# Performance work log

Measured on AMD Instinct MI355X. Metric: run time of the kernel, lower is better.

The kernel has to match this reference:

```python
import math
import jax, jax.numpy as jnp
import numpy as np

B, C, F, W_FRAMES = 1, 8, 1024, 512
H = 16                      # num_heads
D = F // H                  # head dim = 64
ROPE_DIM = D // 2           # 32: only first half of head dim is rotated
EXP = 4                     # ffn expansion
EPS = 1e-5
MAX_FREQ = 10.0             # rotary-embedding-torch default


def frame_norm(x, g, b):
    # LayerNorm over the feature axis (axis=2) of (b, c, F, w)
    mu = jnp.mean(x, axis=2, keepdims=True)
    var = jnp.mean(jnp.square(x - mu), axis=2, keepdims=True)
    xn = (x - mu) * jax.lax.rsqrt(var + EPS)
    return xn * g[None, None, :, None] + b[None, None, :, None]


def mc_linear(x, w_pw):
    # per-channel pointwise linear: out[b,c,f,w] = sum_g W[c,f,g] x[b,c,g,w]
    return jnp.einsum('bcgw,cfg->bcfw', x, w_pw)


def apply_rope(t, freqs_seq):
    # t: (b, c, H, w, d); freqs_seq: (w, rot_dim)
    rot_dim = freqs_seq.shape[-1]
    t_rot, t_pass = t[..., :rot_dim], t[..., rot_dim:]
    cos, sin = jnp.cos(freqs_seq), jnp.sin(freqs_seq)
    x1, x2 = t_rot[..., 0::2], t_rot[..., 1::2]
    rh = jnp.stack([-x2, x1], axis=-1).reshape(t_rot.shape)  # interleaved rotate_half
    return jnp.concatenate([t_rot * cos + rh * sin, t_pass], axis=-1)


def attention(x, w_q, w_o, rope_freqs):
    b, c, f, w = x.shape
    # NOTE: source uses q_proj for q, k AND v (k_proj/v_proj unused)
    p = mc_linear(x, w_q)                                    # (b,c,F,w)
    t = p.transpose(0, 1, 3, 2).reshape(b, c, w, H, D).transpose(0, 1, 3, 2, 4)  # (b,c,H,w,d)
    pos = jnp.arange(w, dtype=t.dtype)
    freqs_seq = jnp.repeat(pos[:, None] * rope_freqs[None, :], 2, axis=-1)  # (w, rot_dim)
    q = apply_rope(t, freqs_seq)
    k = apply_rope(t, freqs_seq)
    v = t
    scores = jnp.einsum('bchqd,bchkd->bchqk', q, k) / math.sqrt(f)  # scaled by sqrt(features)!
    a = jax.nn.softmax(scores, axis=-1)
    o = jnp.einsum('bchqk,bchkd->bchqd', a, v)
    o = o.transpose(0, 1, 3, 2, 4).reshape(b, c, w, f).transpose(0, 1, 3, 2)  # (b,c,F,w)
    return mc_linear(o, w_o)


def setup_inputs() -> dict:
    key = jax.random.key(0)
    ks = jax.random.split(key, 8)
    s = 1.0 / math.sqrt(F)
    se = 1.0 / math.sqrt(F * EXP)
    x = jax.random.normal(ks[0], (B, C, F, W_FRAMES), dtype=jnp.float32)
    w_q = jax.random.uniform(ks[1], (C, F, F), jnp.float32, -s, s)
    w_o = jax.random.uniform(ks[2], (C, F, F), jnp.float32, -s, s)
    w1 = jax.random.uniform(ks[3], (C, F * EXP, F), jnp.float32, -s, s)
    w2 = jax.random.uniform(ks[4], (C, F, F * EXP), jnp.float32, -se, se)
    rope_freqs = jnp.linspace(1.0, MAX_FREQ / 2, ROPE_DIM // 2, dtype=jnp.float32) * math.pi
    return {
        'x': x,
        'norm1_g': jnp.ones((F,), jnp.float32), 'norm1_b': jnp.zeros((F,), jnp.float32),
        'w_q': w_q, 'w_o': w_o, 'rope_freqs': rope_freqs,
        'norm2_g': jnp.ones((F,), jnp.float32), 'norm2_b': jnp.zeros((F,), jnp.float32),
        'w1': w1, 'w2': w2,
    }


def reference(x, norm1_g, norm1_b, w_q, w_o, rope_freqs, norm2_g, norm2_b, w1, w2):
    # FrameTransformerEncoder, eval mode (dropout = identity)
    z = frame_norm(x, norm1_g, norm1_b)
    x = x + attention(z, w_q, w_o, rope_freqs)
    z = frame_norm(x, norm2_g, norm2_b)
    z = mc_linear(jax.nn.gelu(mc_linear(z, w1), approximate=False), w2)
    return x + z
```

## Files before the change

### kernel.cpp

```cpp
#include <hip/hip_runtime.h>
#include <math.h>

#define CC 8
#define FF 1024
#define WW 512
#define HH 16
#define DD 64
#define FE 4096
#define EPS_ 1e-5f

typedef __attribute__((ext_vector_type(8))) short bf16x8;
typedef __attribute__((ext_vector_type(4))) float f32x4;

static __device__ __forceinline__ unsigned short f2bf(float f) {
    unsigned u = __float_as_uint(f);
    u += 0x7fffu + ((u >> 16) & 1u);
    return (unsigned short)(u >> 16);
}
static __device__ __forceinline__ float bf2f(unsigned short h) {
    return __uint_as_float(((unsigned)h) << 16);
}
static __device__ __forceinline__ float gelu_exact(float v) {
    return 0.5f * v * (1.0f + erff(v * 0.70710678118654752f));
}
static __device__ __forceinline__ unsigned cvt_pk_bf16(float lo, float hi) {
    unsigned r;
    asm("v_cvt_pk_bf16_f32 %0, %1, %2" : "=v"(r) : "v"(lo), "v"(hi));
    return r;
}

typedef const __attribute__((address_space(1))) unsigned int* gas_p;
typedef __attribute__((address_space(3))) unsigned int* las_p;
static __device__ __forceinline__ void gload_lds16(const void* g, void* l) {
    __builtin_amdgcn_global_load_lds((gas_p)g, (las_p)l, 16, 0, 0);
}

__global__ __launch_bounds__(256) void fn_stats_k(
    const float* __restrict__ x, float2* __restrict__ part)
{
    int c  = blockIdx.z;
    int w0 = blockIdx.x * 64;
    int f0 = blockIdx.y * 128;
    int t  = threadIdx.x, wl = t & 63, fg = t >> 6;
    const float* xc = x + (size_t)c * FF * WW;

    float s = 0.f, q = 0.f;
    #pragma unroll 8
    for (int i = 0; i < 32; i++) {
        int f = f0 + fg + 4 * i;
        float v = xc[(size_t)f * WW + w0 + wl];
        s += v; q += v * v;
    }
    __shared__ float ss[4][64], sq_[4][64];
    ss[fg][wl] = s; sq_[fg][wl] = q;
    __syncthreads();
    if (fg == 0) {
        float S = 0.f, Q = 0.f;
        #pragma unroll
        for (int j = 0; j < 4; j++) { S += ss[j][wl]; Q += sq_[j][wl]; }
        part[((size_t)c * WW + w0 + wl) * 8 + blockIdx.y] = make_float2(S, Q);
    }
}

__global__ __launch_bounds__(256) void fn_apply_k(
    const float* __restrict__ x, const float2* __restrict__ part,
    const float* __restrict__ g, const float* __restrict__ b,
    unsigned short* __restrict__ zt)
{
    int c  = blockIdx.z;
    int w0 = blockIdx.x * 64;
    int f0 = blockIdx.y * 64;
    int t  = threadIdx.x, wl = t & 63, fg = t >> 6;

    __shared__ float smu[64], srv[64];
    __shared__ float sT[64][65];

    if (t < 64) {
        float S = 0.f, Q = 0.f;
        #pragma unroll
        for (int fs = 0; fs < 8; fs++) {
            float2 v = part[((size_t)c * WW + w0 + t) * 8 + fs];
            S += v.x; Q += v.y;
        }
        float mu  = S * (1.f / FF);
        float var = Q * (1.f / FF) - mu * mu;
        smu[t] = mu;
        srv[t] = rsqrtf(var + EPS_);
    }
    const float* xc = x + (size_t)c * FF * WW;
    #pragma unroll
    for (int i = 0; i < 16; i++) {
        int fl = fg * 16 + i;
        sT[fl][wl] = xc[(size_t)(f0 + fl) * WW + w0 + wl];
    }
    __syncthreads();

    unsigned short* ztc = zt + (size_t)c * WW * FF;
    float gv = g[f0 + wl], bv = b[f0 + wl];
    #pragma unroll
    for (int i = 0; i < 16; i++) {
        int wr = fg * 16 + i;
        ztc[(size_t)(w0 + wr) * FF + f0 + wl] =
            f2bf((sT[wl][wr] - smu[wr]) * srv[wr] * gv + bv);
    }
}

template<int BM, int MINW>
__global__ __launch_bounds__(256, MINW) void gemm_v6_k(
    const float* __restrict__ A, const unsigned short* __restrict__ Bt,
    float* __restrict__ Outf, unsigned short* __restrict__ Outb,
    const float* __restrict__ Add, int M, int K, int mode)
{
    constexpr int L  = BM / 16;
    constexpr int MI = BM / 32;
    constexpr int AP = 72;

    int bid = blockIdx.x;
    int c   = bid & 7;
    int rem = bid >> 3;
    int nt  = rem & 3;
    int mt  = rem >> 2;
    int m0  = mt * BM, n0 = nt * 128;
    const float*          Ac = A  + (size_t)c * M * K;
    const unsigned short* Bc = Bt + ((size_t)c * 512 + n0) * K;

    __shared__ unsigned short sA[2][BM * AP];
    __shared__ unsigned short sB[2][128 * 64];

    int t    = threadIdx.x;
    int lane = t & 63;
    int wid  = t >> 6;
    int frl  = lane & 15, fgr = lane >> 4;
    int WM   = (wid >> 1) * (MI * 16);
    int WN   = (wid & 1) * 64;

    f32x4 acc[MI][4];
    #pragma unroll
    for (int i = 0; i < MI; i++)
        #pragma unroll
        for (int j = 0; j < 4; j++) acc[i][j] = (f32x4){0.f, 0.f, 0.f, 0.f};

    int arow = t >> 4;
    int acol = (t & 15) * 4;
    float4 ar[L];

    int bro   = lane >> 3;
    int bslot = (lane & 7) ^ bro;

    auto loadA = [&](int k0) {
        #pragma unroll
        for (int p = 0; p < L; p++)
            ar[p] = *reinterpret_cast<const float4*>(
                Ac + (size_t)(m0 + p * 16 + arow) * K + k0 + acol);
    };
    auto cvtWriteA = [&](int buf) {
        #pragma unroll
        for (int p = 0; p < L; p++) {
            uint2 u;
            u.x = cvt_pk_bf16(ar[p].x, ar[p].y);
            u.y = cvt_pk_bf16(ar[p].z, ar[p].w);
            *reinterpret_cast<uint2*>(&sA[buf][(p * 16 + arow) * AP + acol]) = u;
        }
    };
    auto stageB = [&](int buf, int k0) {
        #pragma unroll
        for (int r = 0; r < 4; r++) {
            int rbase = wid * 32 + r * 8;
            gload_lds16(Bc + (size_t)(rbase + bro) * K + k0 + bslot * 8,
                        &sB[buf][rbase * 64]);
        }
    };

    loadA(0);
    asm volatile("s_waitcnt vmcnt(0)" ::: "memory");
    cvtWriteA(0);
    stageB(0, 0);

    int NT = K >> 6;
    for (int kt = 0; kt < NT; ++kt) {
        int  cur  = kt & 1;
        bool more = (kt + 1 < NT);

        if (more) loadA((kt + 1) << 6);
        if (more) {
            if constexpr (BM == 128)
                asm volatile("s_waitcnt vmcnt(8)" ::: "memory");
            else
                asm volatile("s_waitcnt vmcnt(4)" ::: "memory");
        } else {
            asm volatile("s_waitcnt vmcnt(0)" ::: "memory");
        }
        asm volatile("s_waitcnt lgkmcnt(0)" ::: "memory");
        __builtin_amdgcn_sched_barrier(0);
        __builtin_amdgcn_s_barrier();

        if (more) stageB(cur ^ 1, (kt + 1) << 6);

        #pragma unroll
        for (int ks = 0; ks < 2; ks++) {
            bf16x8 af[MI], bfv[4];
            #pragma unroll
            for (int mi = 0; mi < MI; mi++)
                af[mi] = *reinterpret_cast<const bf16x8*>(
                    &sA[cur][(WM + mi * 16 + frl) * AP + ks * 32 + fgr * 8]);
            #pragma unroll
            for (int ni = 0; ni < 4; ni++) {
                int row  = WN + ni * 16 + frl;
                int slot = ((ks << 2) | fgr) ^ (frl & 7);
                bfv[ni] = *reinterpret_cast<const bf16x8*>(
                    &sB[cur][row * 64 + slot * 8]);
            }
            #pragma unroll
            for (int mi = 0; mi < MI; mi++)
                #pragma unroll
                for (int ni = 0; ni < 4; ni++)
                    acc[mi][ni] = __builtin_amdgcn_mfma_f32_16x16x32_bf16(
                        af[mi], bfv[ni], acc[mi][ni], 0, 0, 0);
        }

        if (more) {
            asm volatile("s_waitcnt vmcnt(4)" ::: "memory");
            __builtin_amdgcn_sched_barrier(0);
            cvtWriteA(cur ^ 1);
        }
    }

    if (mode == 1) {
        #pragma unroll
        for (int mi = 0; mi < MI; mi++)
            #pragma unroll
            for (int ni = 0; ni < 4; ni++) {
                int mrow = m0 + WM + mi * 16 + fgr * 4;
                int ncol = n0 + WN + ni * 16 + frl;
                #pragma unroll
                for (int r = 0; r < 4; r++) {
                    size_t o = ((size_t)c * M + mrow + r) * 512 + ncol;
                    Outf[o] = acc[mi][ni][r] + Add[o];
                }
            }
    } else {
        bool gel = (mode == 2);
        #pragma unroll
        for (int mi = 0; mi < MI; mi++)
            #pragma unroll
            for (int ni = 0; ni < 4; ni++) {
                f32x4 v = acc[mi][ni];
                if (gel) {
                    v[0] = gelu_exact(v[0]); v[1] = gelu_exact(v[1]);
                    v[2] = gelu_exact(v[2]); v[3] = gelu_exact(v[3]);
                }
                int mrow = m0 + WM + mi * 16 + fgr * 4;
                int ncol = n0 + WN + ni * 16 + frl;
                ushort4 h;
                h.x = f2bf(v[0]); h.y = f2bf(v[1]);
                h.z = f2bf(v[2]); h.w = f2bf(v[3]);
                *reinterpret_cast<ushort4*>(
                    &Outb[((size_t)c * 512 + ncol) * M + mrow]) = h;
            }
    }
}

__global__ __launch_bounds__(256) void attn_mfma_k(
    const unsigned short* __restrict__ pt, const float* __restrict__ fr,
    unsigned short* __restrict__ ot)
{
    int ch = blockIdx.y;
    int c  = ch >> 4, h = ch & 15;
    int q0 = blockIdx.x * 64;
    int t  = threadIdx.x;
    int lane = t & 63;
    int wid  = t >> 6;
    int frl  = lane & 15, fgr = lane >> 4;

    const unsigned short* base = pt + (size_t)c * WW * FF + h * DD;

    __shared__ unsigned short Qs[64 * 72];
    __shared__ unsigned short Ks[64 * 72];
    __shared__ unsigned short Vt[64 * 72];
    __shared__ unsigned short Ps[4 * 16 * 72];

    {
        int kr = t >> 3, d0 = (t & 7) * 8;
        #pragma unroll
        for (int r = 0; r < 2; r++) {
            int row = kr + r * 32;
            int w   = q0 + row;
            bf16x8 v = *reinterpret_cast<const bf16x8*>(&base[(size_t)w * FF + d0]);
            bf16x8 o;
            if (d0 < 32) {
                #pragma unroll
                for (int j = 0; j < 8; j += 2) {
                    float x1 = bf2f((unsigned short)v[j]);
                    float x2 = bf2f((unsigned short)v[j + 1]);
                    float sn, cs;
                    __sincosf((float)w * fr[(d0 + j) >> 1], &sn, &cs);
                    o[j]     = (short)f2bf(x1 * cs - x2 * sn);
                    o[j + 1] = (short)f2bf(x2 * cs + x1 * sn);
                }
            } else o = v;
            *reinterpret_cast<bf16x8*>(&Qs[row * 72 + d0]) = o;
        }
    }

    f32x4 oacc[4];
    float m_[4], l_[4];
    #pragma unroll
    for (int i = 0; i < 4; i++) {
        oacc[i] = (f32x4){0.f, 0.f, 0.f, 0.f};
        m_[i] = -1e30f; l_[i] = 0.f;
    }
    unsigned short* myP = &Ps[wid * 16 * 72];
    int wq0 = wid * 16;

    for (int k0 = 0; k0 < WW; k0 += 64) {
        __syncthreads();
        {
            int kr = t >> 3, d0 = (t & 7) * 8;
            #pragma unroll
            for (int r = 0; r < 2; r++) {
                int row = kr + r * 32;
                int w   = k0 + row;
                bf16x8 v = *reinterpret_cast<const bf16x8*>(&base[(size_t)w * FF + d0]);
                bf16x8 o;
                if (d0 < 32) {
                    #pragma unroll
                    for (int j = 0; j < 8; j += 2) {
                        float x1 = bf2f((unsigned short)v[j]);
                        float x2 = bf2f((unsigned short)v[j + 1]);
                        float sn, cs;
                        __sincosf((float)w * fr[(d0 + j) >> 1], &sn, &cs);
                        o[j]     = (short)f2bf(x1 * cs - x2 * sn);
                        o[j + 1] = (short)f2bf(x2 * cs + x1 * sn);
                    }
                } else o = v;
                *reinterpret_cast<bf16x8*>(&Ks[row * 72 + d0]) = o;
            }
        }
        {
            int d  = t & 63;
            int kb = (t >> 6) * 8;
            #pragma unroll
            for (int r = 0; r < 2; r++) {
                int kk = kb + r * 32;
                bf16x8 o;
                #pragma unroll
                for (int j = 0; j < 8; j++)
                    o[j] = (short)base[(size_t)(k0 + kk + j) * FF + d];
                *reinterpret_cast<bf16x8*>(&Vt[d * 72 + kk]) = o;
            }
        }
        __syncthreads();

        f32x4 s[4];
        #pragma unroll
        for (int nt = 0; nt < 4; nt++) s[nt] = (f32x4){0.f, 0.f, 0.f, 0.f};
        bf16x8 aq0 = *reinterpret_cast<const bf16x8*>(&Qs[(wq0 + frl) * 72 + fgr * 8]);
        bf16x8 aq1 = *reinterpret_cast<const bf16x8*>(&Qs[(wq0 + frl) * 72 + 32 + fgr * 8]);
        #pragma unroll
        for (int nt = 0; nt < 4; nt++) {
            bf16x8 b0 = *reinterpret_cast<const bf16x8*>(&Ks[(nt * 16 + frl) * 72 + fgr * 8]);
            bf16x8 b1 = *reinterpret_cast<const bf16x8*>(&Ks[(nt * 16 + frl) * 72 + 32 + fgr * 8]);
            s[nt] = __builtin_amdgcn_mfma_f32_16x16x32_bf16(aq0, b0, s[nt], 0, 0, 0);
            s[nt] = __builtin_amdgcn_mfma_f32_16x16x32_bf16(aq1, b1, s[nt], 0, 0, 0);
        }

        #pragma unroll
        for (int r = 0; r < 4; r++) {
            float sv[4];
            #pragma unroll
            for (int nt = 0; nt < 4; nt++) sv[nt] = s[nt][r] * (1.f / 32.f);
            float mx = fmaxf(fmaxf(sv[0], sv[1]), fmaxf(sv[2], sv[3]));
            mx = fmaxf(mx, __shfl_xor(mx, 1, 64));
            mx = fmaxf(mx, __shfl_xor(mx, 2, 64));
            mx = fmaxf(mx, __shfl_xor(mx, 4, 64));
            mx = fmaxf(mx, __shfl_xor(mx, 8, 64));
            float mn    = fmaxf(m_[r], mx);
            float scale = __expf(m_[r] - mn);
            float rs = 0.f;
            #pragma unroll
            for (int nt = 0; nt < 4; nt++) {
                float p = __expf(sv[nt] - mn);
                myP[(fgr * 4 + r) * 72 + nt * 16 + frl] = f2bf(p);
                rs += p;
            }
            rs += __shfl_xor(rs, 1, 64);
            rs += __shfl_xor(rs, 2, 64);
            rs += __shfl_xor(rs, 4, 64);
            rs += __shfl_xor(rs, 8, 64);
            l_[r] = l_[r] * scale + rs;
            m_[r] = mn;
            #pragma unroll
            for (int dt = 0; dt < 4; dt++) oacc[dt][r] *= scale;
        }

        bf16x8 ap0 = *reinterpret_cast<const bf16x8*>(&myP[frl * 72 + fgr * 8]);
        bf16x8 ap1 = *reinterpret_cast<const bf16x8*>(&myP[frl * 72 + 32 + fgr * 8]);
        #pragma unroll
        for (int dt = 0; dt < 4; dt++) {
            bf16x8 b0 = *reinterpret_cast<const bf16x8*>(&Vt[(dt * 16 + frl) * 72 + fgr * 8]);
            bf16x8 b1 = *reinterpret_cast<const bf16x8*>(&Vt[(dt * 16 + frl) * 72 + 32 + fgr * 8]);
            oacc[dt] = __builtin_amdgcn_mfma_f32_16x16x32_bf16(ap0, b0, oacc[dt], 0, 0, 0);
            oacc[dt] = __builtin_amdgcn_mfma_f32_16x16x32_bf16(ap1, b1, oacc[dt], 0, 0, 0);
        }
    }

    unsigned short* ob = ot + (size_t)c * WW * FF + h * DD;
    #pragma unroll
    for (int r = 0; r < 4; r++) {
        float inv = 1.f / l_[r];
        int w = q0 + wq0 + fgr * 4 + r;
        #pragma unroll
        for (int dt = 0; dt < 4; dt++)
            ob[(size_t)w * FF + dt * 16 + frl] = f2bf(oacc[dt][r] * inv);
    }
}

extern "C" void kernel_launch(void* const* d_in, const int* in_sizes, int n_in,
                              void* d_out, int out_size, void* d_ws, size_t ws_size,
                              hipStream_t stream)
{
    const float* x  = (const float*)d_in[0];
    const float* g1 = (const float*)d_in[1];
    const float* b1 = (const float*)d_in[2];
    const float* wq = (const float*)d_in[3];
    const float* wo = (const float*)d_in[4];
    const float* fr = (const float*)d_in[5];
    const float* g2 = (const float*)d_in[6];
    const float* b2 = (const float*)d_in[7];
    const float* w1 = (const float*)d_in[8];
    const float* w2 = (const float*)d_in[9];

    const size_t SZ = (size_t)CC * FF * WW;
    char* wsb = (char*)d_ws;
    unsigned short* zt  = (unsigned short*)(wsb);
    unsigned short* ptb = (unsigned short*)(wsb + 2 * SZ);
    unsigned short* otb = (unsigned short*)(wsb + 4 * SZ);
    float*          x2  = (float*)        (wsb + 6 * SZ);
    unsigned short* h1t = (unsigned short*)(wsb + 10 * SZ);
    float2*         prt = (float2*)       (wsb + 18 * SZ);

    dim3 b256(256);
    dim3 gst(WW / 64, FF / 128, CC);
    dim3 gap(WW / 64, FF / 64, CC);

    fn_stats_k<<<gst, b256, 0, stream>>>(x, prt);
    fn_apply_k<<<gap, b256, 0, stream>>>(x, prt, g1, b1, zt);
    gemm_v6_k<64, 3><<<dim3(512), b256, 0, stream>>>(
        wq, zt, nullptr, ptb, nullptr, FF, FF, 0);
    attn_mfma_k<<<dim3(WW / 64, CC * HH), b256, 0, stream>>>(ptb, fr, otb);
    gemm_v6_k<64, 3><<<dim3(512), b256, 0, stream>>>(
        wo, otb, x2, nullptr, x, FF, FF, 1);
    fn_stats_k<<<gst, b256, 0, stream>>>(x2, prt);
    fn_apply_k<<<gap, b256, 0, stream>>>(x2, prt, g2, b2, zt);
    gemm_v6_k<128, 2><<<dim3(1024), b256, 0, stream>>>(
        w1, zt, nullptr, h1t, nullptr, FE, FF, 2);
    gemm_v6_k<64, 3><<<dim3(512), b256, 0, stream>>>(
        w2, h1t, (float*)d_out, nullptr, x2, FF, FE, 1);
}
```

Before: 265.1 us.

## Switch GEMM inner loop to 32x32x16 bf16 MFMA with XOR-swizzled A tile

Replaces the 16x16x32 MFMA tiling in the shared GEMM kernel with 32x32x16 bf16 MFMA instructions, so each wave computes larger fragments and issues fewer instructions and LDS fragment reads per unit of work. The padded A shared-memory tile (stride 72) becomes an unpadded stride-64 layout with an XOR swizzle that matches the B tile, which removes padding and is meant to avoid bank conflicts. The epilogue is rewritten for the 32x32 accumulator layout. The 16-float accumulators may raise register pressure, and the new output write pattern changes coalescing.

```diff
diff --git a/kernel.cpp b/kernel.cpp
--- a/kernel.cpp
+++ b/kernel.cpp
@@ -11,6 +11,7 @@
 
 typedef __attribute__((ext_vector_type(8))) short bf16x8;
 typedef __attribute__((ext_vector_type(4))) float f32x4;
+typedef __attribute__((ext_vector_type(16))) float f32x16;
 
 static __device__ __forceinline__ unsigned short f2bf(float f) {
     unsigned u = __float_as_uint(f);
@@ -106,14 +107,13 @@
 }
 
 template<int BM, int MINW>
-__global__ __launch_bounds__(256, MINW) void gemm_v6_k(
+__global__ __launch_bounds__(256, MINW) void gemm_v7_k(
     const float* __restrict__ A, const unsigned short* __restrict__ Bt,
     float* __restrict__ Outf, unsigned short* __restrict__ Outb,
     const float* __restrict__ Add, int M, int K, int mode)
 {
     constexpr int L  = BM / 16;
-    constexpr int MI = BM / 32;
-    constexpr int AP = 72;
+    constexpr int MF = BM / 64;
 
     int bid = blockIdx.x;
     int c   = bid & 7;
@@ -124,24 +124,28 @@
     const float*          Ac = A  + (size_t)c * M * K;
     const unsigned short* Bc = Bt + ((size_t)c * 512 + n0) * K;
 
-    __shared__ unsigned short sA[2][BM * AP];
+    __shared__ unsigned short sA[2][BM * 64];
     __shared__ unsigned short sB[2][128 * 64];
 
     int t    = threadIdx.x;
     int lane = t & 63;
     int wid  = t >> 6;
-    int frl  = lane & 15, fgr = lane >> 4;
-    int WM   = (wid >> 1) * (MI * 16);
+    int l31  = lane & 31, l5 = lane >> 5;
+    int r7   = l31 & 7;
+    int WM   = (wid >> 1) * (BM / 2);
     int WN   = (wid & 1) * 64;
 
-    f32x4 acc[MI][4];
+    f32x16 acc[MF][2];
     #pragma unroll
-    for (int i = 0; i < MI; i++)
-        #pragma unroll
-        for (int j = 0; j < 4; j++) acc[i][j] = (f32x4){0.f, 0.f, 0.f, 0.f};
+    for (int i = 0; i < MF; i++)
+        #pragma unroll
+        for (int j = 0; j < 2; j++)
+            #pragma unroll
+            for (int e = 0; e < 16; e++) acc[i][j][e] = 0.f;
 
     int arow = t >> 4;
     int acol = (t & 15) * 4;
+    int awz  = (((acol >> 3) ^ (arow & 7)) << 3) + (acol & 7);
     float4 ar[L];
 
     int bro   = lane >> 3;
@@ -159,7 +163,7 @@
             uint2 u;
             u.x = cvt_pk_bf16(ar[p].x, ar[p].y);
             u.y = cvt_pk_bf16(ar[p].z, ar[p].w);
-            *reinterpret_cast<uint2*>(&sA[buf][(p * 16 + arow) * AP + acol]) = u;
+            *reinterpret_cast<uint2*>(&sA[buf][(p * 16 + arow) * 64 + awz]) = u;
         }
     };
     auto stageB = [&](int buf, int k0) {
@@ -197,25 +201,23 @@
         if (more) stageB(cur ^ 1, (kt + 1) << 6);
 
         #pragma unroll
-        for (int ks = 0; ks < 2; ks++) {
-            bf16x8 af[MI], bfv[4];
-            #pragma unroll
-            for (int mi = 0; mi < MI; mi++)
-                af[mi] = *reinterpret_cast<const bf16x8*>(
-                    &sA[cur][(WM + mi * 16 + frl) * AP + ks * 32 + fgr * 8]);
-            #pragma unroll
-            for (int ni = 0; ni < 4; ni++) {
-                int row  = WN + ni * 16 + frl;
-                int slot = ((ks << 2) | fgr) ^ (frl & 7);
-                bfv[ni] = *reinterpret_cast<const bf16x8*>(
-                    &sB[cur][row * 64 + slot * 8]);
-            }
-            #pragma unroll
-            for (int mi = 0; mi < MI; mi++)
+        for (int ksf = 0; ksf < 4; ksf++) {
+            int gx = (((ksf * 2 + l5) ^ r7) << 3);
+            bf16x8 af[MF], bfv[2];
+            #pragma unroll
+            for (int mf = 0; mf < MF; mf++)
+                af[mf] = *reinterpret_cast<const bf16x8*>(
+                    &sA[cur][(WM + mf * 32 + l31) * 64 + gx]);
+            #pragma unroll
+            for (int nf = 0; nf < 2; nf++)
+                bfv[nf] = *reinterpret_cast<const bf16x8*>(
+                    &sB[cur][(WN + nf * 32 + l31) * 64 + gx]);
+            #pragma unroll
+            for (int mf = 0; mf < MF; mf++)
                 #pragma unroll
-                for (int ni = 0; ni < 4; ni++)
-                    acc[mi][ni] = __builtin_amdgcn_mfma_f32_16x16x32_bf16(
-                        af[mi], bfv[ni], acc[mi][ni], 0, 0, 0);
+                for (int nf = 0; nf < 2; nf++)
+                    acc[mf][nf] = __builtin_amdgcn_mfma_f32_32x32x16_bf16(
+                        af[mf], bfv[nf], acc[mf][nf], 0, 0, 0);
         }
 
         if (more) {
@@ -227,35 +229,44 @@
 
     if (mode == 1) {
         #pragma unroll
-        for (int mi = 0; mi < MI; mi++)
-            #pragma unroll
-            for (int ni = 0; ni < 4; ni++) {
-                int mrow = m0 + WM + mi * 16 + fgr * 4;
-                int ncol = n0 + WN + ni * 16 + frl;
+        for (int mf = 0; mf < MF; mf++)
+            #pragma unroll
+            for (int nf = 0; nf < 2; nf++) {
+                int ncol = n0 + WN + nf * 32 + l31;
+                int mb   = m0 + WM + mf * 32 + l5 * 4;
                 #pragma unroll
-                for (int r = 0; r < 4; r++) {
-                    size_t o = ((size_t)c * M + mrow + r) * 512 + ncol;
-                    Outf[o] = acc[mi][ni][r] + Add[o];
-                }
+                for (int g = 0; g < 4; g++)
+                    #pragma unroll
+                    for (int j = 0; j < 4; j++) {
+                        int row = mb + g * 8 + j;
+                        size_t o = ((size_t)c * M + row) * 512 + ncol;
+                        Outf[o] = acc[mf][nf][g * 4 + j] + Add[o];
+                    }
             }
     } else {
         bool gel = (mode == 2);
         #pragma unroll
-        for (int mi = 0; mi < MI; mi++)
-            #pragma unroll
-            for (int ni = 0; ni < 4; ni++) {
-                f32x4 v = acc[mi][ni];
-                if (gel) {
-                    v[0] = gelu_exact(v[0]); v[1] = gelu_exact(v[1]);
-                    v[2] = gelu_exact(v[2]); v[3] = gelu_exact(v[3]);
+        for (int mf = 0; mf < MF; mf++)
+            #pragma unroll
+            for (int nf = 0; nf < 2; nf++) {
+                int ncol = n0 + WN + nf * 32 + l31;
+                int mb   = m0 + WM + mf * 32 + l5 * 4;
+                #pragma unroll
+                for (int g = 0; g < 4; g++) {
+                    float v0 = acc[mf][nf][g * 4 + 0];
+                    float v1 = acc[mf][nf][g * 4 + 1];
+                    float v2 = acc[mf][nf][g * 4 + 2];
+                    float v3 = acc[mf][nf][g * 4 + 3];
+                    if (gel) {
+                        v0 = gelu_exact(v0); v1 = gelu_exact(v1);
+                        v2 = gelu_exact(v2); v3 = gelu_exact(v3);
+                    }
+                    ushort4 h;
+                    h.x = f2bf(v0); h.y = f2bf(v1);
+                    h.z = f2bf(v2); h.w = f2bf(v3);
+                    *reinterpret_cast<ushort4*>(
+                        &Outb[((size_t)c * 512 + ncol) * M + mb + g * 8]) = h;
                 }
-                int mrow = m0 + WM + mi * 16 + fgr * 4;
-                int ncol = n0 + WN + ni * 16 + frl;
-                ushort4 h;
-                h.x = f2bf(v[0]); h.y = f2bf(v[1]);
-                h.z = f2bf(v[2]); h.w = f2bf(v[3]);
-                *reinterpret_cast<ushort4*>(
-                    &Outb[((size_t)c * 512 + ncol) * M + mrow]) = h;
             }
     }
 }
@@ -445,15 +456,15 @@
 
     fn_stats_k<<<gst, b256, 0, stream>>>(x, prt);
     fn_apply_k<<<gap, b256, 0, stream>>>(x, prt, g1, b1, zt);
-    gemm_v6_k<64, 3><<<dim3(512), b256, 0, stream>>>(
+    gemm_v7_k<64, 3><<<dim3(512), b256, 0, stream>>>(
         wq, zt, nullptr, ptb, nullptr, FF, FF, 0);
     attn_mfma_k<<<dim3(WW / 64, CC * HH), b256, 0, stream>>>(ptb, fr, otb);
-    gemm_v6_k<64, 3><<<dim3(512), b256, 0, stream>>>(
+    gemm_v7_k<64, 3><<<dim3(512), b256, 0, stream>>>(
         wo, otb, x2, nullptr, x, FF, FF, 1);
     fn_stats_k<<<gst, b256, 0, stream>>>(x2, prt);
     fn_apply_k<<<gap, b256, 0, stream>>>(x2, prt, g2, b2, zt);
-    gemm_v6_k<128, 2><<<dim3(1024), b256, 0, stream>>>(
+    gemm_v7_k<128, 2><<<dim3(1024), b256, 0, stream>>>(
         w1, zt, nullptr, h1t, nullptr, FE, FF, 2);
-    gemm_v6_k<64, 3><<<dim3(512), b256, 0, stream>>>(
+    gemm_v7_k<64, 3><<<dim3(512), b256, 0, stream>>>(
         w2, h1t, (float*)d_out, nullptr, x2, FF, FE, 1);
 }
```

New measurement: 302.8 us. +14.2%, slower.

## Add dedicated 128x256-tile GEMM kernel for the W1 FFN projection

Applied to the files above, without the earlier changes.

Replaces the generic templated GEMM used for the first FFN layer with a specialized kernel that computes a 128x256 output tile per block (4 waves, each 64x128), halving the grid to 512 blocks. Each block loads fp32 weights, converts them to bf16 in registers, and double-buffers both operands in LDS, with B staged via direct global-to-LDS loads. The larger tile increases reuse of the weight and activation tiles, cutting global traffic per FLOP. In exchange it uses many accumulator registers (launch bounds of 2 blocks per CU) and fewer blocks, which may reduce occupancy and latency hiding.

```diff
diff --git a/kernel.cpp b/kernel.cpp
--- a/kernel.cpp
+++ b/kernel.cpp
@@ -258,6 +258,136 @@
                     &Outb[((size_t)c * 512 + ncol) * M + mrow]) = h;
             }
     }
+}
+
+__global__ __launch_bounds__(256, 2) void gemm_w1big_k(
+    const float* __restrict__ A, const unsigned short* __restrict__ Bt,
+    unsigned short* __restrict__ Outb, int M, int K)
+{
+    constexpr int L  = 4;
+    constexpr int G  = 4;
+    constexpr int AP = 40;
+
+    int bid = blockIdx.x;
+    int c   = bid & 7;
+    int rem = bid >> 3;
+    int nt  = rem & 1;
+    int mt  = rem >> 1;
+    int m0  = mt * 128, n0 = nt * 256;
+    const float*          Ac = A  + (size_t)c * M * K;
+    const unsigned short* Bc = Bt + ((size_t)c * 512 + n0) * K;
+
+    __shared__ unsigned short sA[2][128 * AP];
+    __shared__ unsigned short sB[2][256 * 32];
+
+    int t    = threadIdx.x;
+    int lane = t & 63;
+    int wid  = t >> 6;
+    int frl  = lane & 15, fgr = lane >> 4;
+    int WM   = (wid >> 1) * 64;
+    int WN   = (wid & 1) * 128;
+
+    f32x4 acc[4][8];
+    #pragma unroll
+    for (int i = 0; i < 4; i++)
+        #pragma unroll
+        for (int j = 0; j < 8; j++) acc[i][j] = (f32x4){0.f, 0.f, 0.f, 0.f};
+
+    int arow = t >> 3;
+    int acol = (t & 7) * 4;
+    float4 ar[L];
+
+    int bro   = lane >> 2;
+    int bslot = (lane & 3) ^ (bro & 3);
+
+    auto loadA = [&](int k0) {
+        #pragma unroll
+        for (int p = 0; p < L; p++)
+            ar[p] = *reinterpret_cast<const float4*>(
+                Ac + (size_t)(m0 + p * 32 + arow) * K + k0 + acol);
+    };
+    auto cvtWriteA = [&](int buf) {
+        #pragma unroll
+        for (int p = 0; p < L; p++) {
+            uint2 u;
+            u.x = cvt_pk_bf16(ar[p].x, ar[p].y);
+            u.y = cvt_pk_bf16(ar[p].z, ar[p].w);
+            *reinterpret_cast<uint2*>(&sA[buf][(p * 32 + arow) * AP + acol]) = u;
+        }
+    };
+    auto stageB = [&](int buf, int k0) {
+        #pragma unroll
+        for (int r = 0; r < G; r++) {
+            int rbase = wid * 64 + r * 16;
+            gload_lds16(Bc + (size_t)(rbase + bro) * K + k0 + bslot * 8,
+                        &sB[buf][rbase * 32]);
+        }
+    };
+
+    loadA(0);
+    asm volatile("s_waitcnt vmcnt(0)" ::: "memory");
+    cvtWriteA(0);
+    stageB(0, 0);
+
+    int NT = K >> 5;
+    for (int kt = 0; kt < NT; ++kt) {
+        int  cur  = kt & 1;
+        bool more = (kt + 1 < NT);
+
+        if (more) loadA((kt + 1) << 5);
+        if (more)
+            asm volatile("s_waitcnt vmcnt(4)" ::: "memory");
+        else
+            asm volatile("s_waitcnt vmcnt(0)" ::: "memory");
+        asm volatile("s_waitcnt lgkmcnt(0)" ::: "memory");
+        __builtin_amdgcn_sched_barrier(0);
+        __builtin_amdgcn_s_barrier();
+
+        if (more) stageB(cur ^ 1, (kt + 1) << 5);
+
+        {
+            bf16x8 af[4], bfv[8];
+            #pragma unroll
+            for (int mi = 0; mi < 4; mi++)
+                af[mi] = *reinterpret_cast<const bf16x8*>(
+                    &sA[cur][(WM + mi * 16 + frl) * AP + fgr * 8]);
+            #pragma unroll
+            for (int ni = 0; ni < 8; ni++) {
+                int row  = WN + ni * 16 + frl;
+                int slot = fgr ^ (row & 3);
+                bfv[ni] = *reinterpret_cast<const bf16x8*>(
+                    &sB[cur][row * 32 + slot * 8]);
+            }
+            #pragma unroll
+            for (int mi = 0; mi < 4; mi++)
+                #pragma unroll
+                for (int ni = 0; ni < 8; ni++)
+                    acc[mi][ni] = __builtin_amdgcn_mfma_f32_16x16x32_bf16(
+                        af[mi], bfv[ni], acc[mi][ni], 0, 0, 0);
+        }
+
+        if (more) {
+            asm volatile("s_waitcnt vmcnt(4)" ::: "memory");
+            __builtin_amdgcn_sched_barrier(0);
+            cvtWriteA(cur ^ 1);
+        }
+    }
+
+    #pragma unroll
+    for (int mi = 0; mi < 4; mi++)
+        #pragma unroll
+        for (int ni = 0; ni < 8; ni++) {
+            f32x4 v = acc[mi][ni];
+            v[0] = gelu_exact(v[0]); v[1] = gelu_exact(v[1]);
+            v[2] = gelu_exact(v[2]); v[3] = gelu_exact(v[3]);
+            int mrow = m0 + WM + mi * 16 + fgr * 4;
+            int ncol = n0 + WN + ni * 16 + frl;
+            ushort4 h;
+            h.x = f2bf(v[0]); h.y = f2bf(v[1]);
+            h.z = f2bf(v[2]); h.w = f2bf(v[3]);
+            *reinterpret_cast<ushort4*>(
+                &Outb[((size_t)c * 512 + ncol) * M + mrow]) = h;
+        }
 }
 
 __global__ __launch_bounds__(256) void attn_mfma_k(
@@ -452,8 +582,7 @@
         wo, otb, x2, nullptr, x, FF, FF, 1);
     fn_stats_k<<<gst, b256, 0, stream>>>(x2, prt);
     fn_apply_k<<<gap, b256, 0, stream>>>(x2, prt, g2, b2, zt);
-    gemm_v6_k<128, 2><<<dim3(1024), b256, 0, stream>>>(
-        w1, zt, nullptr, h1t, nullptr, FE, FF, 2);
+    gemm_w1big_k<<<dim3(512), b256, 0, stream>>>(w1, zt, h1t, FE, FF);
     gemm_v6_k<64, 3><<<dim3(512), b256, 0, stream>>>(
         w2, h1t, (float*)d_out, nullptr, x2, FF, FE, 1);
 }
```

Result: no change. 259.9 us, median of 2 (-2.0%).
